# Kernel optimization log

Hardware: AMD Instinct MI355X
Metric: run time of the kernel (lower is better)

## Reference

```python
import jax, jax.numpy as jnp
import numpy as np

D_MODEL = 1024
D_STATE = 256

def setup_inputs() -> dict:
    key = jax.random.key(0)
    k1, k2, k3, k4 = jax.random.split(key, 4)
    x = jax.random.normal(k1, (8, 4096, D_MODEL), dtype=jnp.float32)
    A = jax.random.normal(k2, (D_STATE,), dtype=jnp.float32)
    B = jax.random.normal(k3, (D_STATE, D_MODEL), dtype=jnp.float32) * 0.01
    C = jax.random.normal(k4, (D_MODEL, D_STATE), dtype=jnp.float32) * 0.01
    D = jnp.ones((D_MODEL,), dtype=jnp.float32)
    return {"x": x, "A": A, "B": B, "C": C, "D": D}

def reference(x, A, B, C, D):
    # x: (b, s, d_model)
    a_bar = jnp.exp(-jnp.exp(A))                     # (n,)
    Bx = jnp.einsum('bsd,nd->bsn', x, B)             # (b, s, n) precomputed input drive

    def step(h, bx_t):
        h = a_bar * h + bx_t                          # (b, n)
        return h, h

    h0 = jnp.zeros((x.shape[0], A.shape[0]), dtype=x.dtype)
    # scan over time axis: move seq to leading axis
    _, hs = jax.lax.scan(step, h0, jnp.swapaxes(Bx, 0, 1))  # hs: (s, b, n)
    hs = jnp.swapaxes(hs, 0, 1)                      # (b, s, n)
    y = jnp.einsum('bsn,dn->bsd', hs, C) + D * x     # (b, s, d_model)
    return y
```

## Files before the change

kernel.cpp:

```cpp
#include <hip/hip_runtime.h>
#include <cstdint>
#include <cstddef>


typedef __attribute__((ext_vector_type(8))) _Float16 half8;
typedef __attribute__((ext_vector_type(4))) float f32x4;

template<int N, int K, bool FUSE>
__global__ __launch_bounds__(256) void gemm_nt(
    const float* __restrict__ A, const float* __restrict__ Bm,
    float* __restrict__ out, const float* __restrict__ Dv,
    const float* __restrict__ X)
{
  constexpr int BM = 128, BN = 128, BK = 32;
  constexpr int LDT = 40;
  __shared__ __align__(16) _Float16 lA[BM * LDT];
  __shared__ __align__(16) _Float16 lB[BN * LDT];

  const int tid  = threadIdx.x;
  const int lane = tid & 63;
  const int wave = tid >> 6;
  const int wm   = (wave & 1) * 64;
  const int wn   = (wave >> 1) * 64;
  const int quad = lane >> 4;
  const int l16  = lane & 15;

  const long blockM = (long)blockIdx.x * BM;
  const long blockN = (long)blockIdx.y * BN;

  f32x4 acc[4][4];
  #pragma unroll
  for (int i = 0; i < 4; i++)
    #pragma unroll
    for (int j = 0; j < 4; j++)
      acc[i][j] = (f32x4){0.f, 0.f, 0.f, 0.f};

  for (int k0 = 0; k0 < K; k0 += BK) {
    #pragma unroll
    for (int i = 0; i < 2; i++) {
      const int ch  = tid + i * 256;
      const int row = ch >> 2;
      const int kc  = (ch & 3) * 8;

      const float* ga = A + (blockM + row) * (long)K + (k0 + kc);
      float4 a0 = *(const float4*)ga;
      float4 a1 = *(const float4*)(ga + 4);
      half8 pa;
      pa[0] = (_Float16)a0.x; pa[1] = (_Float16)a0.y;
      pa[2] = (_Float16)a0.z; pa[3] = (_Float16)a0.w;
      pa[4] = (_Float16)a1.x; pa[5] = (_Float16)a1.y;
      pa[6] = (_Float16)a1.z; pa[7] = (_Float16)a1.w;
      *(half8*)&lA[row * LDT + kc] = pa;

      const float* gb = Bm + (blockN + row) * (long)K + (k0 + kc);
      float4 b0 = *(const float4*)gb;
      float4 b1 = *(const float4*)(gb + 4);
      half8 pb;
      pb[0] = (_Float16)b0.x; pb[1] = (_Float16)b0.y;
      pb[2] = (_Float16)b0.z; pb[3] = (_Float16)b0.w;
      pb[4] = (_Float16)b1.x; pb[5] = (_Float16)b1.y;
      pb[6] = (_Float16)b1.z; pb[7] = (_Float16)b1.w;
      *(half8*)&lB[row * LDT + kc] = pb;
    }
    __syncthreads();

    half8 af[4], bf[4];
    #pragma unroll
    for (int mt = 0; mt < 4; mt++)
      af[mt] = *(const half8*)&lA[(wm + mt * 16 + l16) * LDT + quad * 8];
    #pragma unroll
    for (int nt = 0; nt < 4; nt++)
      bf[nt] = *(const half8*)&lB[(wn + nt * 16 + l16) * LDT + quad * 8];

    #pragma unroll
    for (int mt = 0; mt < 4; mt++)
      #pragma unroll
      for (int nt = 0; nt < 4; nt++)
        acc[mt][nt] = __builtin_amdgcn_mfma_f32_16x16x32_f16(
            af[mt], bf[nt], acc[mt][nt], 0, 0, 0);
    __syncthreads();
  }

  #pragma unroll
  for (int mt = 0; mt < 4; mt++) {
    #pragma unroll
    for (int nt = 0; nt < 4; nt++) {
      const long col = blockN + wn + nt * 16 + l16;
      #pragma unroll
      for (int r = 0; r < 4; r++) {
        const long row = blockM + wm + mt * 16 + quad * 4 + r;
        float v = acc[mt][nt][r];
        if (FUSE) v += Dv[col] * X[row * (long)N + col];
        out[row * (long)N + col] = v;
      }
    }
  }
}


__global__ __launch_bounds__(256) void scan_local(
    float* __restrict__ Bx, const float* __restrict__ Ap,
    float* __restrict__ E)
{
  const int n  = threadIdx.x;
  const int bc = blockIdx.x;
  const float al = expf(-expf(Ap[n]));
  size_t base = (size_t)bc * 64 * 256 + n;
  float h = 0.f;
  #pragma unroll 8
  for (int t = 0; t < 64; t++) {
    const size_t i = base + (size_t)t * 256;
    h = al * h + Bx[i];
    Bx[i] = h;
  }
  E[(size_t)bc * 256 + n] = h;
}

__global__ __launch_bounds__(256) void scan_prefix(
    const float* __restrict__ E, const float* __restrict__ Ap,
    float* __restrict__ carry)
{
  const int n = threadIdx.x;
  const int b = blockIdx.x;
  const float al = expf(-expf(Ap[n]));
  float aL = al;
  #pragma unroll
  for (int i = 0; i < 6; i++) aL *= aL;
  float run = 0.f;
  for (int c = 0; c < 64; c++) {
    const size_t idx = ((size_t)b * 64 + c) * 256 + n;
    carry[idx] = run;
    run = aL * run + E[idx];
  }
}

__global__ __launch_bounds__(256) void scan_fix(
    float* __restrict__ Bx, const float* __restrict__ Ap,
    const float* __restrict__ carry)
{
  const int n  = threadIdx.x;
  const int bc = blockIdx.x;
  const float al = expf(-expf(Ap[n]));
  const float car = carry[(size_t)bc * 256 + n];
  size_t base = (size_t)bc * 64 * 256 + n;
  float p = al;
  #pragma unroll 8
  for (int t = 0; t < 64; t++) {
    const size_t i = base + (size_t)t * 256;
    Bx[i] = fmaf(p, car, Bx[i]);
    p *= al;
  }
}

extern "C" void kernel_launch(void* const* d_in, const int* in_sizes, int n_in,
                              void* d_out, int out_size, void* d_ws, size_t ws_size,
                              hipStream_t stream) {
  const float* x  = (const float*)d_in[0];
  const float* Ap = (const float*)d_in[1];
  const float* Bp = (const float*)d_in[2];
  const float* Cp = (const float*)d_in[3];
  const float* Dp = (const float*)d_in[4];
  float* y = (float*)d_out;

  float* Bx    = (float*)d_ws;
  float* E     = Bx + (size_t)32768 * 256;
  float* carry = E + (size_t)512 * 256;

  gemm_nt<256, 1024, false><<<dim3(256, 2), 256, 0, stream>>>(
      x, Bp, Bx, nullptr, nullptr);

  scan_local <<<512, 256, 0, stream>>>(Bx, Ap, E);
  scan_prefix<<<8,   256, 0, stream>>>(E, Ap, carry);
  scan_fix   <<<512, 256, 0, stream>>>(Bx, Ap, carry);

  gemm_nt<1024, 256, true><<<dim3(256, 8), 256, 0, stream>>>(
      Bx, Cp, y, Dp, x);
}
```

Baseline: 360.1 us.

## Store intermediate Bx as fp16, double-buffer GEMMs, widen first GEMM tile

The intermediate Bx/hs buffer is now stored in fp16 instead of fp32, roughly halving its read and write traffic across the GEMM, scan and output stages. The first GEMM uses a 64x256 tile so each block covers all 256 state columns and x is read only once. Both GEMMs use double-buffered LDS with register prefetch so global loads overlap the MFMA work. The scan is restructured so the first pass only computes chunk end states and the second pass recomputes the recurrence with the carry, avoiding one read-modify-write pass. Rounding the recurrence input and output to fp16 adds error that could matter for accuracy.

```diff
diff --git a/kernel.cpp b/kernel.cpp
--- a/kernel.cpp
+++ b/kernel.cpp
@@ -6,16 +6,165 @@
 typedef __attribute__((ext_vector_type(8))) _Float16 half8;
 typedef __attribute__((ext_vector_type(4))) float f32x4;
 
-template<int N, int K, bool FUSE>
-__global__ __launch_bounds__(256) void gemm_nt(
-    const float* __restrict__ A, const float* __restrict__ Bm,
-    float* __restrict__ out, const float* __restrict__ Dv,
-    const float* __restrict__ X)
-{
-  constexpr int BM = 128, BN = 128, BK = 32;
+__device__ inline half8 cvt8(float4 a, float4 b) {
+  half8 h;
+  h[0] = (_Float16)a.x; h[1] = (_Float16)a.y;
+  h[2] = (_Float16)a.z; h[3] = (_Float16)a.w;
+  h[4] = (_Float16)b.x; h[5] = (_Float16)b.y;
+  h[6] = (_Float16)b.z; h[7] = (_Float16)b.w;
+  return h;
+}
+
+__global__ __launch_bounds__(256) void gemm_bx(
+    const float* __restrict__ x, const float* __restrict__ Bp,
+    _Float16* __restrict__ Bxh)
+{
   constexpr int LDT = 40;
-  __shared__ __align__(16) _Float16 lA[BM * LDT];
-  __shared__ __align__(16) _Float16 lB[BN * LDT];
+  __shared__ __align__(16) _Float16 lA[2][64 * LDT];
+  __shared__ __align__(16) _Float16 lB[2][256 * LDT];
+
+  const int tid  = threadIdx.x;
+  const int lane = tid & 63;
+  const int wave = tid >> 6;
+  const int wn   = wave * 64;
+  const int quad = lane >> 4;
+  const int l16  = lane & 15;
+  const long blockM = (long)blockIdx.x * 64;
+
+  const int arow = tid >> 2, akc = (tid & 3) * 8;
+  const float* gA = x + (blockM + arow) * 1024 + akc;
+  int brow[4], bkc[4];
+  const float* gB[4];
+  #pragma unroll
+  for (int i = 0; i < 4; i++) {
+    const int ch = tid + i * 256;
+    brow[i] = ch >> 2; bkc[i] = (ch & 3) * 8;
+    gB[i] = Bp + brow[i] * 1024 + bkc[i];
+  }
+
+  float4 ra0, ra1, rb0[4], rb1[4];
+  ra0 = *(const float4*)gA; ra1 = *(const float4*)(gA + 4);
+  #pragma unroll
+  for (int i = 0; i < 4; i++) {
+    rb0[i] = *(const float4*)gB[i]; rb1[i] = *(const float4*)(gB[i] + 4);
+  }
+  *(half8*)&lA[0][arow * LDT + akc] = cvt8(ra0, ra1);
+  #pragma unroll
+  for (int i = 0; i < 4; i++)
+    *(half8*)&lB[0][brow[i] * LDT + bkc[i]] = cvt8(rb0[i], rb1[i]);
+  __syncthreads();
+
+  f32x4 acc[4][4];
+  #pragma unroll
+  for (int i = 0; i < 4; i++)
+    #pragma unroll
+    for (int j = 0; j < 4; j++) acc[i][j] = (f32x4){0.f, 0.f, 0.f, 0.f};
+
+  for (int it = 0; it < 32; ++it) {
+    const int cur = it & 1;
+    if (it < 31) {
+      const int k = (it + 1) * 32;
+      ra0 = *(const float4*)(gA + k); ra1 = *(const float4*)(gA + k + 4);
+      #pragma unroll
+      for (int i = 0; i < 4; i++) {
+        rb0[i] = *(const float4*)(gB[i] + k);
+        rb1[i] = *(const float4*)(gB[i] + k + 4);
+      }
+    }
+    half8 af[4], bf[4];
+    #pragma unroll
+    for (int mt = 0; mt < 4; mt++)
+      af[mt] = *(const half8*)&lA[cur][(mt * 16 + l16) * LDT + quad * 8];
+    #pragma unroll
+    for (int nt = 0; nt < 4; nt++)
+      bf[nt] = *(const half8*)&lB[cur][(wn + nt * 16 + l16) * LDT + quad * 8];
+    #pragma unroll
+    for (int mt = 0; mt < 4; mt++)
+      #pragma unroll
+      for (int nt = 0; nt < 4; nt++)
+        acc[mt][nt] = __builtin_amdgcn_mfma_f32_16x16x32_f16(
+            af[mt], bf[nt], acc[mt][nt], 0, 0, 0);
+    if (it < 31) {
+      *(half8*)&lA[cur ^ 1][arow * LDT + akc] = cvt8(ra0, ra1);
+      #pragma unroll
+      for (int i = 0; i < 4; i++)
+        *(half8*)&lB[cur ^ 1][brow[i] * LDT + bkc[i]] = cvt8(rb0[i], rb1[i]);
+    }
+    __syncthreads();
+  }
+
+  #pragma unroll
+  for (int mt = 0; mt < 4; mt++)
+    #pragma unroll
+    for (int nt = 0; nt < 4; nt++) {
+      const int col = wn + nt * 16 + l16;
+      #pragma unroll
+      for (int r = 0; r < 4; r++) {
+        const long row = blockM + mt * 16 + quad * 4 + r;
+        Bxh[row * 256 + col] = (_Float16)acc[mt][nt][r];
+      }
+    }
+}
+
+
+__global__ __launch_bounds__(256) void scan_E(
+    const _Float16* __restrict__ Bxh, const float* __restrict__ Ap,
+    float* __restrict__ E)
+{
+  const int n  = threadIdx.x;
+  const int bc = blockIdx.x;
+  const float al = expf(-expf(Ap[n]));
+  const size_t base = (size_t)bc * 64 * 256 + n;
+  float h = 0.f;
+  #pragma unroll 8
+  for (int t = 0; t < 64; t++)
+    h = fmaf(al, h, (float)Bxh[base + (size_t)t * 256]);
+  E[(size_t)bc * 256 + n] = h;
+}
+
+__global__ __launch_bounds__(256) void scan_prefix(
+    const float* __restrict__ E, const float* __restrict__ Ap,
+    float* __restrict__ carry)
+{
+  const int n = threadIdx.x;
+  const int b = blockIdx.x;
+  const float al = expf(-expf(Ap[n]));
+  float aL = al;
+  #pragma unroll
+  for (int i = 0; i < 6; i++) aL *= aL;
+  float run = 0.f;
+  for (int c = 0; c < 64; c++) {
+    const size_t idx = ((size_t)b * 64 + c) * 256 + n;
+    carry[idx] = run;
+    run = fmaf(aL, run, E[idx]);
+  }
+}
+
+__global__ __launch_bounds__(256) void scan_apply(
+    _Float16* __restrict__ Bxh, const float* __restrict__ Ap,
+    const float* __restrict__ carry)
+{
+  const int n  = threadIdx.x;
+  const int bc = blockIdx.x;
+  const float al = expf(-expf(Ap[n]));
+  float h = carry[(size_t)bc * 256 + n];
+  const size_t base = (size_t)bc * 64 * 256 + n;
+  #pragma unroll 8
+  for (int t = 0; t < 64; t++) {
+    const size_t i = base + (size_t)t * 256;
+    h = fmaf(al, h, (float)Bxh[i]);
+    Bxh[i] = (_Float16)h;
+  }
+}
+
+__global__ __launch_bounds__(256) void gemm_y(
+    const _Float16* __restrict__ hs, const float* __restrict__ Cp,
+    const float* __restrict__ x, const float* __restrict__ Dp,
+    float* __restrict__ y)
+{
+  constexpr int LDT = 40;
+  __shared__ __align__(16) _Float16 lA[2][128 * LDT];
+  __shared__ __align__(16) _Float16 lB[2][128 * LDT];
 
   const int tid  = threadIdx.x;
   const int lane = tid & 63;
@@ -24,132 +173,86 @@
   const int wn   = (wave >> 1) * 64;
   const int quad = lane >> 4;
   const int l16  = lane & 15;
-
-  const long blockM = (long)blockIdx.x * BM;
-  const long blockN = (long)blockIdx.y * BN;
+  const long blockM = (long)blockIdx.x * 128;
+  const long blockN = (long)blockIdx.y * 128;
+
+  int ar[2], ak[2];
+  const _Float16* gA[2];
+  const float* gB[2];
+  #pragma unroll
+  for (int i = 0; i < 2; i++) {
+    const int ch = tid + i * 256;
+    ar[i] = ch >> 2; ak[i] = (ch & 3) * 8;
+    gA[i] = hs + (blockM + ar[i]) * 256 + ak[i];
+    gB[i] = Cp + (blockN + ar[i]) * 256 + ak[i];
+  }
+
+  half8 ha[2]; float4 rb0[2], rb1[2];
+  #pragma unroll
+  for (int i = 0; i < 2; i++) {
+    ha[i]  = *(const half8*)gA[i];
+    rb0[i] = *(const float4*)gB[i];
+    rb1[i] = *(const float4*)(gB[i] + 4);
+  }
+  #pragma unroll
+  for (int i = 0; i < 2; i++) {
+    *(half8*)&lA[0][ar[i] * LDT + ak[i]] = ha[i];
+    *(half8*)&lB[0][ar[i] * LDT + ak[i]] = cvt8(rb0[i], rb1[i]);
+  }
+  __syncthreads();
 
   f32x4 acc[4][4];
   #pragma unroll
   for (int i = 0; i < 4; i++)
     #pragma unroll
-    for (int j = 0; j < 4; j++)
-      acc[i][j] = (f32x4){0.f, 0.f, 0.f, 0.f};
-
-  for (int k0 = 0; k0 < K; k0 += BK) {
-    #pragma unroll
-    for (int i = 0; i < 2; i++) {
-      const int ch  = tid + i * 256;
-      const int row = ch >> 2;
-      const int kc  = (ch & 3) * 8;
-
-      const float* ga = A + (blockM + row) * (long)K + (k0 + kc);
-      float4 a0 = *(const float4*)ga;
-      float4 a1 = *(const float4*)(ga + 4);
-      half8 pa;
-      pa[0] = (_Float16)a0.x; pa[1] = (_Float16)a0.y;
-      pa[2] = (_Float16)a0.z; pa[3] = (_Float16)a0.w;
-      pa[4] = (_Float16)a1.x; pa[5] = (_Float16)a1.y;
-      pa[6] = (_Float16)a1.z; pa[7] = (_Float16)a1.w;
-      *(half8*)&lA[row * LDT + kc] = pa;
-
-      const float* gb = Bm + (blockN + row) * (long)K + (k0 + kc);
-      float4 b0 = *(const float4*)gb;
-      float4 b1 = *(const float4*)(gb + 4);
-      half8 pb;
-      pb[0] = (_Float16)b0.x; pb[1] = (_Float16)b0.y;
-      pb[2] = (_Float16)b0.z; pb[3] = (_Float16)b0.w;
-      pb[4] = (_Float16)b1.x; pb[5] = (_Float16)b1.y;
-      pb[6] = (_Float16)b1.z; pb[7] = (_Float16)b1.w;
-      *(half8*)&lB[row * LDT + kc] = pb;
-    }
-    __syncthreads();
-
+    for (int j = 0; j < 4; j++) acc[i][j] = (f32x4){0.f, 0.f, 0.f, 0.f};
+
+  for (int it = 0; it < 8; ++it) {
+    const int cur = it & 1;
+    if (it < 7) {
+      const int k = (it + 1) * 32;
+      #pragma unroll
+      for (int i = 0; i < 2; i++) {
+        ha[i]  = *(const half8*)(gA[i] + k);
+        rb0[i] = *(const float4*)(gB[i] + k);
+        rb1[i] = *(const float4*)(gB[i] + k + 4);
+      }
+    }
     half8 af[4], bf[4];
     #pragma unroll
     for (int mt = 0; mt < 4; mt++)
-      af[mt] = *(const half8*)&lA[(wm + mt * 16 + l16) * LDT + quad * 8];
+      af[mt] = *(const half8*)&lA[cur][(wm + mt * 16 + l16) * LDT + quad * 8];
     #pragma unroll
     for (int nt = 0; nt < 4; nt++)
-      bf[nt] = *(const half8*)&lB[(wn + nt * 16 + l16) * LDT + quad * 8];
-
+      bf[nt] = *(const half8*)&lB[cur][(wn + nt * 16 + l16) * LDT + quad * 8];
     #pragma unroll
     for (int mt = 0; mt < 4; mt++)
       #pragma unroll
       for (int nt = 0; nt < 4; nt++)
         acc[mt][nt] = __builtin_amdgcn_mfma_f32_16x16x32_f16(
             af[mt], bf[nt], acc[mt][nt], 0, 0, 0);
+    if (it < 7) {
+      #pragma unroll
+      for (int i = 0; i < 2; i++) {
+        *(half8*)&lA[cur ^ 1][ar[i] * LDT + ak[i]] = ha[i];
+        *(half8*)&lB[cur ^ 1][ar[i] * LDT + ak[i]] = cvt8(rb0[i], rb1[i]);
+      }
+    }
     __syncthreads();
   }
 
   #pragma unroll
-  for (int mt = 0; mt < 4; mt++) {
+  for (int mt = 0; mt < 4; mt++)
     #pragma unroll
     for (int nt = 0; nt < 4; nt++) {
       const long col = blockN + wn + nt * 16 + l16;
+      const float dcol = Dp[col];
       #pragma unroll
       for (int r = 0; r < 4; r++) {
         const long row = blockM + wm + mt * 16 + quad * 4 + r;
-        float v = acc[mt][nt][r];
-        if (FUSE) v += Dv[col] * X[row * (long)N + col];
-        out[row * (long)N + col] = v;
-      }
-    }
-  }
-}
-
-
-__global__ __launch_bounds__(256) void scan_local(
-    float* __restrict__ Bx, const float* __restrict__ Ap,
-    float* __restrict__ E)
-{
-  const int n  = threadIdx.x;
-  const int bc = blockIdx.x;
-  const float al = expf(-expf(Ap[n]));
-  size_t base = (size_t)bc * 64 * 256 + n;
-  float h = 0.f;
-  #pragma unroll 8
-  for (int t = 0; t < 64; t++) {
-    const size_t i = base + (size_t)t * 256;
-    h = al * h + Bx[i];
-    Bx[i] = h;
-  }
-  E[(size_t)bc * 256 + n] = h;
-}
-
-__global__ __launch_bounds__(256) void scan_prefix(
-    const float* __restrict__ E, const float* __restrict__ Ap,
-    float* __restrict__ carry)
-{
-  const int n = threadIdx.x;
-  const int b = blockIdx.x;
-  const float al = expf(-expf(Ap[n]));
-  float aL = al;
-  #pragma unroll
-  for (int i = 0; i < 6; i++) aL *= aL;
-  float run = 0.f;
-  for (int c = 0; c < 64; c++) {
-    const size_t idx = ((size_t)b * 64 + c) * 256 + n;
-    carry[idx] = run;
-    run = aL * run + E[idx];
-  }
-}
-
-__global__ __launch_bounds__(256) void scan_fix(
-    float* __restrict__ Bx, const float* __restrict__ Ap,
-    const float* __restrict__ carry)
-{
-  const int n  = threadIdx.x;
-  const int bc = blockIdx.x;
-  const float al = expf(-expf(Ap[n]));
-  const float car = carry[(size_t)bc * 256 + n];
-  size_t base = (size_t)bc * 64 * 256 + n;
-  float p = al;
-  #pragma unroll 8
-  for (int t = 0; t < 64; t++) {
-    const size_t i = base + (size_t)t * 256;
-    Bx[i] = fmaf(p, car, Bx[i]);
-    p *= al;
-  }
+        y[row * 1024 + col] = acc[mt][nt][r] + dcol * x[row * 1024 + col];
+      }
+    }
 }
 
 extern "C" void kernel_launch(void* const* d_in, const int* in_sizes, int n_in,
@@ -162,17 +265,13 @@
   const float* Dp = (const float*)d_in[4];
   float* y = (float*)d_out;
 
-  float* Bx    = (float*)d_ws;
-  float* E     = Bx + (size_t)32768 * 256;
-  float* carry = E + (size_t)512 * 256;
-
-  gemm_nt<256, 1024, false><<<dim3(256, 2), 256, 0, stream>>>(
-      x, Bp, Bx, nullptr, nullptr);
-
-  scan_local <<<512, 256, 0, stream>>>(Bx, Ap, E);
-  scan_prefix<<<8,   256, 0, stream>>>(E, Ap, carry);
-  scan_fix   <<<512, 256, 0, stream>>>(Bx, Ap, carry);
-
-  gemm_nt<1024, 256, true><<<dim3(256, 8), 256, 0, stream>>>(
-      Bx, Cp, y, Dp, x);
-}
+  _Float16* Bxh  = (_Float16*)d_ws;
+  float*    E    = (float*)((char*)d_ws + (size_t)32768 * 256 * 2);
+  float*    carry = E + (size_t)512 * 256;
+
+  gemm_bx   <<<512, 256, 0, stream>>>(x, Bp, Bxh);
+  scan_E    <<<512, 256, 0, stream>>>(Bxh, Ap, E);
+  scan_prefix<<<8,  256, 0, stream>>>(E, Ap, carry);
+  scan_apply<<<512, 256, 0, stream>>>(Bxh, Ap, carry);
+  gemm_y<<<dim3(256, 8), 256, 0, stream>>>(Bxh, Cp, x, Dp, y);
+}
```

Result: slower. 367.8 us (+2.1%).
